# Optimization experiments

Hardware: AMD Instinct MI355X
Metric: run time of the kernel (lower is better)

Reference implementation:

```python
import jax, jax.numpy as jnp
import numpy as np

N_NODES = 100000
N_EDGES = 1600000
N_GRAPHS = 128
IN_FEATS = 128
OUT_FEATS = 64


def setup_inputs() -> dict:
    key = jax.random.key(0)
    k1, k2, k3, k4, k5, k6 = jax.random.split(key, 6)
    features = jax.random.normal(k1, (N_NODES, IN_FEATS), jnp.float32)
    src = jax.random.randint(k2, (N_EDGES,), 0, N_NODES, dtype=jnp.int32)
    dst = jax.random.randint(k3, (N_EDGES,), 0, N_NODES, dtype=jnp.int32)
    graph_ids = jnp.sort(jax.random.randint(k4, (N_NODES,), 0, N_GRAPHS, dtype=jnp.int32))
    # Xavier-uniform init as in DGL GraphConv
    lim1 = float(np.sqrt(6.0 / (IN_FEATS + IN_FEATS)))
    lim2 = float(np.sqrt(6.0 / (IN_FEATS + OUT_FEATS)))
    W1 = jax.random.uniform(k5, (IN_FEATS, IN_FEATS), jnp.float32, -lim1, lim1)
    W2 = jax.random.uniform(k6, (IN_FEATS, OUT_FEATS), jnp.float32, -lim2, lim2)
    b1 = jnp.zeros((IN_FEATS,), jnp.float32)
    b2 = jnp.zeros((OUT_FEATS,), jnp.float32)
    return {"features": features, "W1": W1, "b1": b1, "W2": W2, "b2": b2,
            "src": src, "dst": dst, "graph_ids": graph_ids, "num_graphs": N_GRAPHS}


def _graph_conv(x, W, b, src, dst, n_nodes):
    # DGL GraphConv, norm='both': D_dst^{-1/2} A D_src^{-1/2} X W + b
    ones = jnp.ones(src.shape, x.dtype)
    deg_out = jax.ops.segment_sum(ones, src, num_segments=n_nodes)
    deg_in = jax.ops.segment_sum(ones, dst, num_segments=n_nodes)
    norm_src = jax.lax.rsqrt(jnp.maximum(deg_out, 1.0))  # [N]
    norm_dst = jax.lax.rsqrt(jnp.maximum(deg_in, 1.0))   # [N]
    h = (x * norm_src[:, None]) @ W                       # dense transform first
    agg = jax.ops.segment_sum(h[src], dst, num_segments=n_nodes)  # spmm-style scatter-add
    return agg * norm_dst[:, None] + b


def reference(features, W1, b1, W2, b2, src, dst, graph_ids, num_graphs):
    n = features.shape[0]
    h = jax.nn.relu(_graph_conv(features, W1, b1, src, dst, n))
    h = jax.nn.relu(_graph_conv(h, W2, b2, src, dst, n))
    # dgl.mean_nodes: per-graph mean over nodes
    sums = jax.ops.segment_sum(h, graph_ids, num_segments=num_graphs)
    counts = jax.ops.segment_sum(jnp.ones((n, 1), h.dtype), graph_ids, num_segments=num_graphs)
    return sums / jnp.maximum(counts, 1.0)
```

## Files before the change

### kernel.cpp

```cpp
#include <hip/hip_runtime.h>
#include <hip/hip_bf16.h>


#define NPP_SHIFT 9
#define NPP 512
#define MAXP 256
#define NB 512

typedef __attribute__((ext_vector_type(8))) short frag8;
typedef __attribute__((ext_vector_type(4))) float f32x4;

__launch_bounds__(256)
__global__ void passA_count(const int* __restrict__ src, const int* __restrict__ dst,
                            int E, int P, int* __restrict__ counts_src,
                            int* __restrict__ counts_dst) {
    __shared__ int h1[MAXP], h2[MAXP];
    int tid = threadIdx.x;
    for (int i = tid; i < P; i += 256) { h1[i] = 0; h2[i] = 0; }
    __syncthreads();
    int per_block = (E + NB - 1) / NB;
    int e0 = blockIdx.x * per_block;
    int e1 = min(e0 + per_block, E);
    for (int e = e0 + tid; e < e1; e += 256) {
        atomicAdd(&h1[src[e] >> NPP_SHIFT], 1);
        atomicAdd(&h2[dst[e] >> NPP_SHIFT], 1);
    }
    __syncthreads();
    for (int i = tid; i < P; i += 256) {
        counts_src[(size_t)blockIdx.x * P + i] = h1[i];
        counts_dst[(size_t)blockIdx.x * P + i] = h2[i];
    }
}

__launch_bounds__(1024)
__global__ void scanB(const int* __restrict__ counts, int* __restrict__ offs,
                      int* __restrict__ ptot, int P) {
    __shared__ int s[1024];
    int tid = threadIdx.x;
    int p = blockIdx.x % P;
    int st = blockIdx.x / P;
    const int* c = counts + (size_t)st * NB * P;
    int v = (tid < NB) ? c[(size_t)tid * P + p] : 0;
    s[tid] = v;
    __syncthreads();
    for (int off = 1; off < 1024; off <<= 1) {
        int t = (tid >= off) ? s[tid - off] : 0;
        __syncthreads();
        s[tid] += t;
        __syncthreads();
    }
    if (tid < NB) offs[(size_t)st * NB * P + (size_t)tid * P + p] = s[tid] - v;
    if (tid == 1023) ptot[st * P + p] = s[1023];
}

__launch_bounds__(256)
__global__ void passC_scatter(const int* __restrict__ src, const int* __restrict__ dst,
                              int E, int P, const int* __restrict__ offs,
                              const int* __restrict__ ptot, int* __restrict__ pbase,
                              int* __restrict__ ebuf_src, int2* __restrict__ ebuf_dst) {
    __shared__ int cur1[MAXP], cur2[MAXP], sc[256];
    int tid = threadIdx.x;
    int v = (tid < P) ? ptot[tid] : 0;
    sc[tid] = v;
    __syncthreads();
    for (int off = 1; off < 256; off <<= 1) {
        int t = (tid >= off) ? sc[tid - off] : 0;
        __syncthreads();
        sc[tid] += t;
        __syncthreads();
    }
    int base0 = sc[tid] - v;
    if (tid < P) {
        cur1[tid] = base0 + offs[(size_t)blockIdx.x * P + tid];
        if (blockIdx.x == 0) pbase[tid] = base0;
    }
    __syncthreads();
    v = (tid < P) ? ptot[P + tid] : 0;
    sc[tid] = v;
    __syncthreads();
    for (int off = 1; off < 256; off <<= 1) {
        int t = (tid >= off) ? sc[tid - off] : 0;
        __syncthreads();
        sc[tid] += t;
        __syncthreads();
    }
    int base1 = sc[tid] - v;
    if (tid < P) {
        cur2[tid] = base1 + offs[(size_t)NB * P + (size_t)blockIdx.x * P + tid];
        if (blockIdx.x == 0) pbase[P + tid] = base1;
    }
    __syncthreads();
    int per_block = (E + NB - 1) / NB;
    int e0 = blockIdx.x * per_block;
    int e1 = min(e0 + per_block, E);
    for (int e = e0 + tid; e < e1; e += 256) {
        int s = src[e];
        int d = dst[e];
        int pos1 = atomicAdd(&cur1[s >> NPP_SHIFT], 1);
        ebuf_src[pos1] = s;
        int pos2 = atomicAdd(&cur2[d >> NPP_SHIFT], 1);
        ebuf_dst[pos2] = make_int2(d, s);
    }
}

__launch_bounds__(512)
__global__ void passD_build(const int* __restrict__ ebuf_src, const int2* __restrict__ ebuf_dst,
                            const int* __restrict__ ptot, const int* __restrict__ pbase,
                            float* __restrict__ norm_src, int* __restrict__ row_start,
                            int* __restrict__ csr_src, int N, int E, int P) {
    __shared__ int hs[NPP], hd[NPP], sc[NPP];
    int tid = threadIdx.x;
    int p = blockIdx.x;
    int node_lo = p << NPP_SHIFT;
    int nl = min(NPP, N - node_lo);
    hs[tid] = 0;
    hd[tid] = 0;
    __syncthreads();
    int nsrc = ptot[p];
    int base_s = pbase[p];
    for (int i = tid; i < nsrc; i += 512)
        atomicAdd(&hs[ebuf_src[base_s + i] - node_lo], 1);
    int ndst = ptot[P + p];
    int base_d = pbase[P + p];
    for (int i = tid; i < ndst; i += 512)
        atomicAdd(&hd[ebuf_dst[base_d + i].x - node_lo], 1);
    __syncthreads();
    if (tid < nl) norm_src[node_lo + tid] = rsqrtf((float)max(hs[tid], 1));
    int myh = hd[tid];
    sc[tid] = myh;
    __syncthreads();
    for (int off = 1; off < 512; off <<= 1) {
        int t = (tid >= off) ? sc[tid - off] : 0;
        __syncthreads();
        sc[tid] += t;
        __syncthreads();
    }
    int row0 = base_d + sc[tid] - myh;
    if (tid < nl) row_start[node_lo + tid] = row0;
    if (p == P - 1 && tid == 0) row_start[N] = E;
    __syncthreads();
    hd[tid] = row0;
    __syncthreads();
    for (int i = tid; i < ndst; i += 512) {
        int2 r = ebuf_dst[base_d + i];
        int pos = atomicAdd(&hd[r.x - node_lo], 1);
        csr_src[pos] = r.y;
    }
}

template <int COLS, bool BF16IN>
__launch_bounds__(256)
__global__ void gemm_mfma(const void* __restrict__ xin, const float* __restrict__ w,
                          const float* __restrict__ norm,
                          __hip_bfloat16* __restrict__ out, int n) {
    constexpr int NT = COLS / 16;
    __shared__ short wlds[4 * NT * 64 * 8];
    const int tid = threadIdx.x;
    for (int i = tid; i < 128 * COLS / 4; i += 256) {
        int k = (i * 4) / COLS;
        int n0 = (i * 4) % COLS;
        float4 wv = reinterpret_cast<const float4*>(w)[i];
        int c = k >> 5, q = (k >> 3) & 3, j = k & 7;
        float vals[4] = {wv.x, wv.y, wv.z, wv.w};
#pragma unroll
        for (int u = 0; u < 4; ++u) {
            int nn = n0 + u;
            int t = nn >> 4;
            int ln = (q << 4) | (nn & 15);
            union { __hip_bfloat16 b; short s; } cv;
            cv.b = __float2bfloat16(vals[u]);
            wlds[(((c * NT + t) << 6) | ln) * 8 + j] = cv.s;
        }
    }
    __syncthreads();

    const int lane = tid & 63;
    const int wid = tid >> 6;
    const int m = lane & 15;
    const int q = lane >> 4;
    const int ntiles = (n + 15) >> 4;
    const frag8* wfr = reinterpret_cast<const frag8*>(wlds);

    for (int wt = blockIdx.x * 4 + wid; wt < ntiles; wt += gridDim.x * 4) {
        const int row = (wt << 4) + m;
        frag8 af[4];
        if (row < n) {
            if constexpr (BF16IN) {
                const frag8* xp = reinterpret_cast<const frag8*>(
                    (const __hip_bfloat16*)xin + (size_t)row * 128);
#pragma unroll
                for (int c = 0; c < 4; ++c) af[c] = xp[c * 4 + q];
            } else {
                const float* xp = (const float*)xin + (size_t)row * 128;
                float nm = norm[row];
#pragma unroll
                for (int c = 0; c < 4; ++c) {
                    int base = c * 32 + q * 8;
                    float4 v0 = *reinterpret_cast<const float4*>(xp + base);
                    float4 v1 = *reinterpret_cast<const float4*>(xp + base + 4);
                    union { frag8 f; short s[8]; } a;
                    union { __hip_bfloat16 b; short s; } cv;
                    cv.b = __float2bfloat16(v0.x * nm); a.s[0] = cv.s;
                    cv.b = __float2bfloat16(v0.y * nm); a.s[1] = cv.s;
                    cv.b = __float2bfloat16(v0.z * nm); a.s[2] = cv.s;
                    cv.b = __float2bfloat16(v0.w * nm); a.s[3] = cv.s;
                    cv.b = __float2bfloat16(v1.x * nm); a.s[4] = cv.s;
                    cv.b = __float2bfloat16(v1.y * nm); a.s[5] = cv.s;
                    cv.b = __float2bfloat16(v1.z * nm); a.s[6] = cv.s;
                    cv.b = __float2bfloat16(v1.w * nm); a.s[7] = cv.s;
                    af[c] = a.f;
                }
            }
        } else {
#pragma unroll
            for (int c = 0; c < 4; ++c) af[c] = frag8{0, 0, 0, 0, 0, 0, 0, 0};
        }
        f32x4 acc[NT] = {};
#pragma unroll
        for (int c = 0; c < 4; ++c)
#pragma unroll
            for (int t = 0; t < NT; ++t)
                acc[t] = __builtin_amdgcn_mfma_f32_16x16x32_bf16(
                    af[c], wfr[(c * NT + t) * 64 + lane], acc[t], 0, 0, 0);
#pragma unroll
        for (int r = 0; r < 4; ++r) {
            int grow = (wt << 4) + q * 4 + r;
            if (grow < n) {
#pragma unroll
                for (int t = 0; t < NT; ++t)
                    out[(size_t)grow * COLS + t * 16 + m] = __float2bfloat16(acc[t][r]);
            }
        }
    }
}

__launch_bounds__(256)
__global__ void spmm1_kernel(const __hip_bfloat16* __restrict__ h,
                             const int* __restrict__ row_start,
                             const int* __restrict__ csr_src,
                             const float* __restrict__ b1,
                             const float* __restrict__ norm_src,
                             uint* __restrict__ out, int n) {
    int gw = (blockIdx.x * blockDim.x + threadIdx.x) >> 6;
    int lane = threadIdx.x & 63;
    if (gw >= n) return;
    int e0 = row_start[gw];
    int e1 = row_start[gw + 1];
    const uint* hp = reinterpret_cast<const uint*>(h);
    float2 acc = {0.f, 0.f};
    int e = e0;
    for (; e + 16 <= e1; e += 16) {
        uint v[16];
#pragma unroll
        for (int j = 0; j < 16; ++j)
            v[j] = hp[(size_t)csr_src[e + j] * 64 + lane];
#pragma unroll
        for (int j = 0; j < 16; ++j) {
            acc.x += __uint_as_float(v[j] << 16);
            acc.y += __uint_as_float(v[j] & 0xffff0000u);
        }
    }
    if (e + 8 <= e1) {
        uint v[8];
#pragma unroll
        for (int j = 0; j < 8; ++j)
            v[j] = hp[(size_t)csr_src[e + j] * 64 + lane];
#pragma unroll
        for (int j = 0; j < 8; ++j) {
            acc.x += __uint_as_float(v[j] << 16);
            acc.y += __uint_as_float(v[j] & 0xffff0000u);
        }
        e += 8;
    }
    if (e + 4 <= e1) {
        uint v[4];
#pragma unroll
        for (int j = 0; j < 4; ++j)
            v[j] = hp[(size_t)csr_src[e + j] * 64 + lane];
#pragma unroll
        for (int j = 0; j < 4; ++j) {
            acc.x += __uint_as_float(v[j] << 16);
            acc.y += __uint_as_float(v[j] & 0xffff0000u);
        }
        e += 4;
    }
    if (e + 2 <= e1) {
        uint v0 = hp[(size_t)csr_src[e] * 64 + lane];
        uint v1 = hp[(size_t)csr_src[e + 1] * 64 + lane];
        acc.x += __uint_as_float(v0 << 16);
        acc.y += __uint_as_float(v0 & 0xffff0000u);
        acc.x += __uint_as_float(v1 << 16);
        acc.y += __uint_as_float(v1 & 0xffff0000u);
        e += 2;
    }
    if (e < e1) {
        uint v0 = hp[(size_t)csr_src[e] * 64 + lane];
        acc.x += __uint_as_float(v0 << 16);
        acc.y += __uint_as_float(v0 & 0xffff0000u);
    }
    float nd = rsqrtf((float)max(e1 - e0, 1));
    float ns = norm_src[gw];
    float2 bb = reinterpret_cast<const float2*>(b1)[lane];
    float ox = fmaxf(fmaf(acc.x, nd, bb.x), 0.f) * ns;
    float oy = fmaxf(fmaf(acc.y, nd, bb.y), 0.f) * ns;
    union { __hip_bfloat16 b; ushort s; } cx, cy;
    cx.b = __float2bfloat16(ox);
    cy.b = __float2bfloat16(oy);
    out[(size_t)gw * 64 + lane] = (uint)cx.s | ((uint)cy.s << 16);
}

__launch_bounds__(256)
__global__ void spmm2_kernel(const __hip_bfloat16* __restrict__ h,
                             const int* __restrict__ row_start,
                             const int* __restrict__ csr_src,
                             const float* __restrict__ b2, ushort* __restrict__ y, int n) {
    int gw = (blockIdx.x * blockDim.x + threadIdx.x) >> 6;
    int lane = threadIdx.x & 63;
    if (gw >= n) return;
    int e0 = row_start[gw];
    int e1 = row_start[gw + 1];
    const ushort* hp = reinterpret_cast<const ushort*>(h);
    float acc = 0.f;
    int e = e0;
    for (; e + 16 <= e1; e += 16) {
        uint v[16];
#pragma unroll
        for (int j = 0; j < 16; ++j)
            v[j] = hp[(size_t)csr_src[e + j] * 64 + lane];
#pragma unroll
        for (int j = 0; j < 16; ++j) acc += __uint_as_float(v[j] << 16);
    }
    if (e + 8 <= e1) {
        uint v[8];
#pragma unroll
        for (int j = 0; j < 8; ++j)
            v[j] = hp[(size_t)csr_src[e + j] * 64 + lane];
#pragma unroll
        for (int j = 0; j < 8; ++j) acc += __uint_as_float(v[j] << 16);
        e += 8;
    }
    if (e + 4 <= e1) {
        uint v[4];
#pragma unroll
        for (int j = 0; j < 4; ++j)
            v[j] = hp[(size_t)csr_src[e + j] * 64 + lane];
#pragma unroll
        for (int j = 0; j < 4; ++j) acc += __uint_as_float(v[j] << 16);
        e += 4;
    }
    if (e + 2 <= e1) {
        uint v0 = hp[(size_t)csr_src[e] * 64 + lane];
        uint v1 = hp[(size_t)csr_src[e + 1] * 64 + lane];
        acc += __uint_as_float(v0 << 16);
        acc += __uint_as_float(v1 << 16);
        e += 2;
    }
    if (e < e1) {
        uint v0 = hp[(size_t)csr_src[e] * 64 + lane];
        acc += __uint_as_float(v0 << 16);
    }
    float nd = rsqrtf((float)max(e1 - e0, 1));
    float val = fmaxf(fmaf(acc, nd, b2[lane]), 0.f);
    union { __hip_bfloat16 b; ushort s; } cv;
    cv.b = __float2bfloat16(val);
    y[(size_t)gw * 64 + lane] = cv.s;
}

__launch_bounds__(256)
__global__ void pool_kernel(const ushort* __restrict__ y, const int* __restrict__ gids,
                            float* __restrict__ out, int n) {
    int g = blockIdx.x;
    int lo = 0, hi = n;
    while (lo < hi) {
        int mid = (lo + hi) >> 1;
        if (gids[mid] < g) lo = mid + 1; else hi = mid;
    }
    int s = lo;
    hi = n;
    while (lo < hi) {
        int mid = (lo + hi) >> 1;
        if (gids[mid] < g + 1) lo = mid + 1; else hi = mid;
    }
    int e = lo;
    int lane = threadIdx.x & 63;
    int wave = threadIdx.x >> 6;
    float acc = 0.f;
    int i = s + wave;
    for (; i + 12 < e; i += 16) {
        uint u0 = y[(size_t)(i + 0) * 64 + lane];
        uint u1 = y[(size_t)(i + 4) * 64 + lane];
        uint u2 = y[(size_t)(i + 8) * 64 + lane];
        uint u3 = y[(size_t)(i + 12) * 64 + lane];
        acc += __uint_as_float(u0 << 16) + __uint_as_float(u1 << 16) +
               __uint_as_float(u2 << 16) + __uint_as_float(u3 << 16);
    }
    for (; i < e; i += 4)
        acc += __uint_as_float((uint)y[(size_t)i * 64 + lane] << 16);
    __shared__ float sbuf[4][64];
    sbuf[wave][lane] = acc;
    __syncthreads();
    if (wave == 0) {
        float v = sbuf[0][lane] + sbuf[1][lane] + sbuf[2][lane] + sbuf[3][lane];
        out[(size_t)g * 64 + lane] = v / fmaxf((float)(e - s), 1.f);
    }
}

extern "C" void kernel_launch(void* const* d_in, const int* in_sizes, int n_in,
                              void* d_out, int out_size, void* d_ws, size_t ws_size,
                              hipStream_t stream) {
    const float* features = (const float*)d_in[0];
    const float* W1 = (const float*)d_in[1];
    const float* b1 = (const float*)d_in[2];
    const float* W2 = (const float*)d_in[3];
    const float* b2 = (const float*)d_in[4];
    const int* src = (const int*)d_in[5];
    const int* dst = (const int*)d_in[6];
    const int* gids = (const int*)d_in[7];
    const int N = in_sizes[7];
    const int E = in_sizes[5];
    const int G = out_size / 64;
    float* out = (float*)d_out;
    const int P = (N + NPP - 1) >> NPP_SHIFT;

    char* ws = (char*)d_ws;
    size_t off = 0;
    auto alloc = [&](size_t bytes) -> void* {
        void* p = ws + off;
        off = (off + bytes + 255) & ~(size_t)255;
        return p;
    };
    int* counts = (int*)alloc((size_t)2 * NB * P * 4);
    int* offs = (int*)alloc((size_t)2 * NB * P * 4);
    int* ptot = (int*)alloc((size_t)2 * P * 4);
    int* pbase = (int*)alloc((size_t)2 * P * 4);
    int* ebuf_src = (int*)alloc((size_t)E * 4);
    int2* ebuf_dst = (int2*)alloc((size_t)E * 8);
    float* norm_src = (float*)alloc((size_t)N * 4);
    int* row_start = (int*)alloc((size_t)(N + 1) * 4);
    int* csr_src = (int*)alloc((size_t)E * 4);
    __hip_bfloat16* h1 = (__hip_bfloat16*)alloc((size_t)N * 128 * 2);
    __hip_bfloat16* x2n = (__hip_bfloat16*)alloc((size_t)N * 128 * 2);
    ushort* y = (ushort*)alloc((size_t)N * 64 * 2);
    __hip_bfloat16* h2 = h1;

    const int B = 256;
    passA_count<<<NB, 256, 0, stream>>>(src, dst, E, P, counts, counts + (size_t)NB * P);
    scanB<<<2 * P, 1024, 0, stream>>>(counts, offs, ptot, P);
    passC_scatter<<<NB, 256, 0, stream>>>(src, dst, E, P, offs, ptot, pbase,
                                          ebuf_src, ebuf_dst);
    passD_build<<<P, 512, 0, stream>>>(ebuf_src, ebuf_dst, ptot, pbase, norm_src, row_start,
                                       csr_src, N, E, P);

    gemm_mfma<128, false><<<768, 256, 0, stream>>>(features, W1, norm_src, h1, N);
    spmm1_kernel<<<(N * 64 + B - 1) / B, B, 0, stream>>>(h1, row_start, csr_src, b1, norm_src,
                                                         (uint*)x2n, N);
    gemm_mfma<64, true><<<768, 256, 0, stream>>>(x2n, W2, nullptr, h2, N);
    spmm2_kernel<<<(N * 64 + B - 1) / B, B, 0, stream>>>(h2, row_start, csr_src, b2, y, N);
    pool_kernel<<<G, 256, 0, stream>>>(y, gids, out, N);
}
```

Measured before the change: 331.8 us.

## Split SpMM rows across two waves and use wave-shuffle scans

The two SpMM kernels now assign two waves per destination row, each accumulating alternate edges, and the partial sums are combined through shared memory before the epilogue. This doubles the number of independent gather streams per row to hide memory latency, at the cost of twice as many waves, a block-level barrier and a shared-memory reduction. Separately, the block-wide Hillis-Steele scans in scanB, passC and passD are replaced by wave-shuffle inclusive scans plus a small per-wave prefix, which removes many barriers. scanB also shrinks from 1024 to 512 threads.

```diff
diff --git a/kernel.cpp b/kernel.cpp
--- a/kernel.cpp
+++ b/kernel.cpp
@@ -9,6 +9,16 @@
 
 typedef __attribute__((ext_vector_type(8))) short frag8;
 typedef __attribute__((ext_vector_type(4))) float f32x4;
+
+__device__ inline int wave_incl_scan(int v) {
+    int lane = threadIdx.x & 63;
+#pragma unroll
+    for (int off = 1; off < 64; off <<= 1) {
+        int t = __shfl_up(v, off);
+        if (lane >= off) v += t;
+    }
+    return v;
+}
 
 __launch_bounds__(256)
 __global__ void passA_count(const int* __restrict__ src, const int* __restrict__ dst,
@@ -32,25 +42,27 @@
     }
 }
 
-__launch_bounds__(1024)
+__launch_bounds__(512)
 __global__ void scanB(const int* __restrict__ counts, int* __restrict__ offs,
                       int* __restrict__ ptot, int P) {
-    __shared__ int s[1024];
-    int tid = threadIdx.x;
+    __shared__ int wsum[8];
+    int tid = threadIdx.x;
+    int wave = tid >> 6;
     int p = blockIdx.x % P;
     int st = blockIdx.x / P;
     const int* c = counts + (size_t)st * NB * P;
-    int v = (tid < NB) ? c[(size_t)tid * P + p] : 0;
-    s[tid] = v;
-    __syncthreads();
-    for (int off = 1; off < 1024; off <<= 1) {
-        int t = (tid >= off) ? s[tid - off] : 0;
-        __syncthreads();
-        s[tid] += t;
-        __syncthreads();
-    }
-    if (tid < NB) offs[(size_t)st * NB * P + (size_t)tid * P + p] = s[tid] - v;
-    if (tid == 1023) ptot[st * P + p] = s[1023];
+    int v = c[(size_t)tid * P + p];
+    int incl = wave_incl_scan(v);
+    if ((tid & 63) == 63) wsum[wave] = incl;
+    __syncthreads();
+    if (tid == 0) {
+        int a = 0;
+#pragma unroll
+        for (int i = 0; i < 8; ++i) { int t = wsum[i]; wsum[i] = a; a += t; }
+        ptot[st * P + p] = a;
+    }
+    __syncthreads();
+    offs[(size_t)st * NB * P + (size_t)tid * P + p] = incl - v + wsum[wave];
 }
 
 __launch_bounds__(256)
@@ -58,33 +70,36 @@
                               int E, int P, const int* __restrict__ offs,
                               const int* __restrict__ ptot, int* __restrict__ pbase,
                               int* __restrict__ ebuf_src, int2* __restrict__ ebuf_dst) {
-    __shared__ int cur1[MAXP], cur2[MAXP], sc[256];
-    int tid = threadIdx.x;
+    __shared__ int cur1[MAXP], cur2[MAXP], wsum[4];
+    int tid = threadIdx.x;
+    int wave = tid >> 6;
     int v = (tid < P) ? ptot[tid] : 0;
-    sc[tid] = v;
-    __syncthreads();
-    for (int off = 1; off < 256; off <<= 1) {
-        int t = (tid >= off) ? sc[tid - off] : 0;
-        __syncthreads();
-        sc[tid] += t;
-        __syncthreads();
-    }
-    int base0 = sc[tid] - v;
+    int incl = wave_incl_scan(v);
+    if ((tid & 63) == 63) wsum[wave] = incl;
+    __syncthreads();
+    if (tid == 0) {
+        int a = 0;
+#pragma unroll
+        for (int i = 0; i < 4; ++i) { int t = wsum[i]; wsum[i] = a; a += t; }
+    }
+    __syncthreads();
+    int base0 = incl - v + wsum[wave];
     if (tid < P) {
         cur1[tid] = base0 + offs[(size_t)blockIdx.x * P + tid];
         if (blockIdx.x == 0) pbase[tid] = base0;
     }
     __syncthreads();
     v = (tid < P) ? ptot[P + tid] : 0;
-    sc[tid] = v;
-    __syncthreads();
-    for (int off = 1; off < 256; off <<= 1) {
-        int t = (tid >= off) ? sc[tid - off] : 0;
-        __syncthreads();
-        sc[tid] += t;
-        __syncthreads();
-    }
-    int base1 = sc[tid] - v;
+    incl = wave_incl_scan(v);
+    if ((tid & 63) == 63) wsum[wave] = incl;
+    __syncthreads();
+    if (tid == 0) {
+        int a = 0;
+#pragma unroll
+        for (int i = 0; i < 4; ++i) { int t = wsum[i]; wsum[i] = a; a += t; }
+    }
+    __syncthreads();
+    int base1 = incl - v + wsum[wave];
     if (tid < P) {
         cur2[tid] = base1 + offs[(size_t)NB * P + (size_t)blockIdx.x * P + tid];
         if (blockIdx.x == 0) pbase[P + tid] = base1;
@@ -108,8 +123,9 @@
                             const int* __restrict__ ptot, const int* __restrict__ pbase,
                             float* __restrict__ norm_src, int* __restrict__ row_start,
                             int* __restrict__ csr_src, int N, int E, int P) {
-    __shared__ int hs[NPP], hd[NPP], sc[NPP];
-    int tid = threadIdx.x;
+    __shared__ int hs[NPP], hd[NPP], wsum[8];
+    int tid = threadIdx.x;
+    int wave = tid >> 6;
     int p = blockIdx.x;
     int node_lo = p << NPP_SHIFT;
     int nl = min(NPP, N - node_lo);
@@ -127,15 +143,16 @@
     __syncthreads();
     if (tid < nl) norm_src[node_lo + tid] = rsqrtf((float)max(hs[tid], 1));
     int myh = hd[tid];
-    sc[tid] = myh;
-    __syncthreads();
-    for (int off = 1; off < 512; off <<= 1) {
-        int t = (tid >= off) ? sc[tid - off] : 0;
-        __syncthreads();
-        sc[tid] += t;
-        __syncthreads();
-    }
-    int row0 = base_d + sc[tid] - myh;
+    int incl = wave_incl_scan(myh);
+    if ((tid & 63) == 63) wsum[wave] = incl;
+    __syncthreads();
+    if (tid == 0) {
+        int a = 0;
+#pragma unroll
+        for (int i = 0; i < 8; ++i) { int t = wsum[i]; wsum[i] = a; a += t; }
+    }
+    __syncthreads();
+    int row0 = base_d + incl - myh + wsum[wave];
     if (tid < nl) row_start[node_lo + tid] = row0;
     if (p == P - 1 && tid == 0) row_start[N] = E;
     __syncthreads();
@@ -241,72 +258,66 @@
                              const float* __restrict__ b1,
                              const float* __restrict__ norm_src,
                              uint* __restrict__ out, int n) {
-    int gw = (blockIdx.x * blockDim.x + threadIdx.x) >> 6;
-    int lane = threadIdx.x & 63;
-    if (gw >= n) return;
-    int e0 = row_start[gw];
-    int e1 = row_start[gw + 1];
-    const uint* hp = reinterpret_cast<const uint*>(h);
+    int tid = threadIdx.x;
+    int wave_g = (blockIdx.x * 256 + tid) >> 6;
+    int gw = wave_g >> 1;
+    int sub = wave_g & 1;
+    int lane = tid & 63;
+    int lwave = tid >> 6;
+    __shared__ float2 sbuf[4][64];
     float2 acc = {0.f, 0.f};
-    int e = e0;
-    for (; e + 16 <= e1; e += 16) {
-        uint v[16];
-#pragma unroll
-        for (int j = 0; j < 16; ++j)
-            v[j] = hp[(size_t)csr_src[e + j] * 64 + lane];
-#pragma unroll
-        for (int j = 0; j < 16; ++j) {
-            acc.x += __uint_as_float(v[j] << 16);
-            acc.y += __uint_as_float(v[j] & 0xffff0000u);
-        }
-    }
-    if (e + 8 <= e1) {
-        uint v[8];
-#pragma unroll
-        for (int j = 0; j < 8; ++j)
-            v[j] = hp[(size_t)csr_src[e + j] * 64 + lane];
-#pragma unroll
-        for (int j = 0; j < 8; ++j) {
-            acc.x += __uint_as_float(v[j] << 16);
-            acc.y += __uint_as_float(v[j] & 0xffff0000u);
-        }
-        e += 8;
-    }
-    if (e + 4 <= e1) {
-        uint v[4];
-#pragma unroll
-        for (int j = 0; j < 4; ++j)
-            v[j] = hp[(size_t)csr_src[e + j] * 64 + lane];
-#pragma unroll
-        for (int j = 0; j < 4; ++j) {
-            acc.x += __uint_as_float(v[j] << 16);
-            acc.y += __uint_as_float(v[j] & 0xffff0000u);
-        }
-        e += 4;
-    }
-    if (e + 2 <= e1) {
-        uint v0 = hp[(size_t)csr_src[e] * 64 + lane];
-        uint v1 = hp[(size_t)csr_src[e + 1] * 64 + lane];
-        acc.x += __uint_as_float(v0 << 16);
-        acc.y += __uint_as_float(v0 & 0xffff0000u);
-        acc.x += __uint_as_float(v1 << 16);
-        acc.y += __uint_as_float(v1 & 0xffff0000u);
-        e += 2;
-    }
-    if (e < e1) {
-        uint v0 = hp[(size_t)csr_src[e] * 64 + lane];
-        acc.x += __uint_as_float(v0 << 16);
-        acc.y += __uint_as_float(v0 & 0xffff0000u);
-    }
-    float nd = rsqrtf((float)max(e1 - e0, 1));
-    float ns = norm_src[gw];
-    float2 bb = reinterpret_cast<const float2*>(b1)[lane];
-    float ox = fmaxf(fmaf(acc.x, nd, bb.x), 0.f) * ns;
-    float oy = fmaxf(fmaf(acc.y, nd, bb.y), 0.f) * ns;
-    union { __hip_bfloat16 b; ushort s; } cx, cy;
-    cx.b = __float2bfloat16(ox);
-    cy.b = __float2bfloat16(oy);
-    out[(size_t)gw * 64 + lane] = (uint)cx.s | ((uint)cy.s << 16);
+    int e0 = 0, e1 = 0;
+    bool active = gw < n;
+    if (active) {
+        e0 = row_start[gw];
+        e1 = row_start[gw + 1];
+        const uint* hp = reinterpret_cast<const uint*>(h);
+        int e = e0 + sub;
+        for (; e + 14 < e1; e += 16) {
+            uint v[8];
+#pragma unroll
+            for (int j = 0; j < 8; ++j)
+                v[j] = hp[(size_t)csr_src[e + 2 * j] * 64 + lane];
+#pragma unroll
+            for (int j = 0; j < 8; ++j) {
+                acc.x += __uint_as_float(v[j] << 16);
+                acc.y += __uint_as_float(v[j] & 0xffff0000u);
+            }
+        }
+        if (e + 6 < e1) {
+            uint v[4];
+#pragma unroll
+            for (int j = 0; j < 4; ++j)
+                v[j] = hp[(size_t)csr_src[e + 2 * j] * 64 + lane];
+#pragma unroll
+            for (int j = 0; j < 4; ++j) {
+                acc.x += __uint_as_float(v[j] << 16);
+                acc.y += __uint_as_float(v[j] & 0xffff0000u);
+            }
+            e += 8;
+        }
+        for (; e < e1; e += 2) {
+            uint v0 = hp[(size_t)csr_src[e] * 64 + lane];
+            acc.x += __uint_as_float(v0 << 16);
+            acc.y += __uint_as_float(v0 & 0xffff0000u);
+        }
+    }
+    sbuf[lwave][lane] = acc;
+    __syncthreads();
+    if (active && sub == 0) {
+        float2 pp = sbuf[lwave ^ 1][lane];
+        acc.x += pp.x;
+        acc.y += pp.y;
+        float nd = rsqrtf((float)max(e1 - e0, 1));
+        float ns = norm_src[gw];
+        float2 bb = reinterpret_cast<const float2*>(b1)[lane];
+        float ox = fmaxf(fmaf(acc.x, nd, bb.x), 0.f) * ns;
+        float oy = fmaxf(fmaf(acc.y, nd, bb.y), 0.f) * ns;
+        union { __hip_bfloat16 b; ushort s; } cx, cy;
+        cx.b = __float2bfloat16(ox);
+        cy.b = __float2bfloat16(oy);
+        out[(size_t)gw * 64 + lane] = (uint)cx.s | ((uint)cy.s << 16);
+    }
 }
 
 __launch_bounds__(256)
@@ -314,56 +325,51 @@
                              const int* __restrict__ row_start,
                              const int* __restrict__ csr_src,
                              const float* __restrict__ b2, ushort* __restrict__ y, int n) {
-    int gw = (blockIdx.x * blockDim.x + threadIdx.x) >> 6;
-    int lane = threadIdx.x & 63;
-    if (gw >= n) return;
-    int e0 = row_start[gw];
-    int e1 = row_start[gw + 1];
-    const ushort* hp = reinterpret_cast<const ushort*>(h);
+    int tid = threadIdx.x;
+    int wave_g = (blockIdx.x * 256 + tid) >> 6;
+    int gw = wave_g >> 1;
+    int sub = wave_g & 1;
+    int lane = tid & 63;
+    int lwave = tid >> 6;
+    __shared__ float sbuf[4][64];
     float acc = 0.f;
-    int e = e0;
-    for (; e + 16 <= e1; e += 16) {
-        uint v[16];
-#pragma unroll
-        for (int j = 0; j < 16; ++j)
-            v[j] = hp[(size_t)csr_src[e + j] * 64 + lane];
-#pragma unroll
-        for (int j = 0; j < 16; ++j) acc += __uint_as_float(v[j] << 16);
-    }
-    if (e + 8 <= e1) {
-        uint v[8];
-#pragma unroll
-        for (int j = 0; j < 8; ++j)
-            v[j] = hp[(size_t)csr_src[e + j] * 64 + lane];
-#pragma unroll
-        for (int j = 0; j < 8; ++j) acc += __uint_as_float(v[j] << 16);
-        e += 8;
-    }
-    if (e + 4 <= e1) {
-        uint v[4];
-#pragma unroll
-        for (int j = 0; j < 4; ++j)
-            v[j] = hp[(size_t)csr_src[e + j] * 64 + lane];
-#pragma unroll
-        for (int j = 0; j < 4; ++j) acc += __uint_as_float(v[j] << 16);
-        e += 4;
-    }
-    if (e + 2 <= e1) {
-        uint v0 = hp[(size_t)csr_src[e] * 64 + lane];
-        uint v1 = hp[(size_t)csr_src[e + 1] * 64 + lane];
-        acc += __uint_as_float(v0 << 16);
-        acc += __uint_as_float(v1 << 16);
-        e += 2;
-    }
-    if (e < e1) {
-        uint v0 = hp[(size_t)csr_src[e] * 64 + lane];
-        acc += __uint_as_float(v0 << 16);
-    }
-    float nd = rsqrtf((float)max(e1 - e0, 1));
-    float val = fmaxf(fmaf(acc, nd, b2[lane]), 0.f);
-    union { __hip_bfloat16 b; ushort s; } cv;
-    cv.b = __float2bfloat16(val);
-    y[(size_t)gw * 64 + lane] = cv.s;
+    int e0 = 0, e1 = 0;
+    bool active = gw < n;
+    if (active) {
+        e0 = row_start[gw];
+        e1 = row_start[gw + 1];
+        const ushort* hp = reinterpret_cast<const ushort*>(h);
+        int e = e0 + sub;
+        for (; e + 14 < e1; e += 16) {
+            uint v[8];
+#pragma unroll
+            for (int j = 0; j < 8; ++j)
+                v[j] = hp[(size_t)csr_src[e + 2 * j] * 64 + lane];
+#pragma unroll
+            for (int j = 0; j < 8; ++j) acc += __uint_as_float(v[j] << 16);
+        }
+        if (e + 6 < e1) {
+            uint v[4];
+#pragma unroll
+            for (int j = 0; j < 4; ++j)
+                v[j] = hp[(size_t)csr_src[e + 2 * j] * 64 + lane];
+#pragma unroll
+            for (int j = 0; j < 4; ++j) acc += __uint_as_float(v[j] << 16);
+            e += 8;
+        }
+        for (; e < e1; e += 2)
+            acc += __uint_as_float((uint)hp[(size_t)csr_src[e] * 64 + lane] << 16);
+    }
+    sbuf[lwave][lane] = acc;
+    __syncthreads();
+    if (active && sub == 0) {
+        acc += sbuf[lwave ^ 1][lane];
+        float nd = rsqrtf((float)max(e1 - e0, 1));
+        float val = fmaxf(fmaf(acc, nd, b2[lane]), 0.f);
+        union { __hip_bfloat16 b; ushort s; } cv;
+        cv.b = __float2bfloat16(val);
+        y[(size_t)gw * 64 + lane] = cv.s;
+    }
 }
 
 __launch_bounds__(256)
@@ -443,18 +449,18 @@
     ushort* y = (ushort*)alloc((size_t)N * 64 * 2);
     __hip_bfloat16* h2 = h1;
 
-    const int B = 256;
     passA_count<<<NB, 256, 0, stream>>>(src, dst, E, P, counts, counts + (size_t)NB * P);
-    scanB<<<2 * P, 1024, 0, stream>>>(counts, offs, ptot, P);
+    scanB<<<2 * P, 512, 0, stream>>>(counts, offs, ptot, P);
     passC_scatter<<<NB, 256, 0, stream>>>(src, dst, E, P, offs, ptot, pbase,
                                           ebuf_src, ebuf_dst);
     passD_build<<<P, 512, 0, stream>>>(ebuf_src, ebuf_dst, ptot, pbase, norm_src, row_start,
                                        csr_src, N, E, P);
 
     gemm_mfma<128, false><<<768, 256, 0, stream>>>(features, W1, norm_src, h1, N);
-    spmm1_kernel<<<(N * 64 + B - 1) / B, B, 0, stream>>>(h1, row_start, csr_src, b1, norm_src,
-                                                         (uint*)x2n, N);
+    int spmm_blocks = (2 * N + 3) / 4;
+    spmm1_kernel<<<spmm_blocks, 256, 0, stream>>>(h1, row_start, csr_src, b1, norm_src,
+                                                  (uint*)x2n, N);
     gemm_mfma<64, true><<<768, 256, 0, stream>>>(x2n, W2, nullptr, h2, N);
-    spmm2_kernel<<<(N * 64 + B - 1) / B, B, 0, stream>>>(h2, row_start, csr_src, b2, y, N);
+    spmm2_kernel<<<spmm_blocks, 256, 0, stream>>>(h2, row_start, csr_src, b2, y, N);
     pool_kernel<<<G, 256, 0, stream>>>(y, gids, out, N);
 }
```

New measurement: 385.5 us. 1.16x slower.
